# Performance work log

Measured on AMD Instinct MI355X. Metric: run time of the kernel, lower is better.

The kernel has to match this reference:

```python
import jax, jax.numpy as jnp
import numpy as np

DIM = 1024
GROUPS = 32
EPS = 1e-5


def setup_inputs() -> dict:
    key = jax.random.key(0)
    ks = jax.random.split(key, 12)
    b, c, h, w = 16, DIM, 32, 32  # h*w must equal DIM for GroupNorm(32, dim) on (b, hw, c)
    x = jax.random.normal(ks[0], (b, c, h, w), dtype=jnp.float32)
    # GroupNorm affine params: num_channels = dim (applied along hw axis, which == dim)
    gamma = jnp.ones((DIM,), dtype=jnp.float32)
    beta = jnp.zeros((DIM,), dtype=jnp.float32)
    init = lambda k: jax.random.normal(k, (DIM, DIM), dtype=jnp.float32) * 0.02
    Wq, Wk, Wv, Wo = init(ks[1]), init(ks[2]), init(ks[3]), init(ks[4])
    bq = jax.random.normal(ks[5], (DIM,), dtype=jnp.float32) * 0.02
    bk = jax.random.normal(ks[6], (DIM,), dtype=jnp.float32) * 0.02
    bv = jax.random.normal(ks[7], (DIM,), dtype=jnp.float32) * 0.02
    bo = jax.random.normal(ks[8], (DIM,), dtype=jnp.float32) * 0.02
    return {"x": x, "gamma": gamma, "beta": beta,
            "Wq": Wq, "bq": bq, "Wk": Wk, "bk": bk,
            "Wv": Wv, "bv": bv, "Wo": Wo, "bo": bo}


def _group_norm(x, gamma, beta):
    # x: (b, N, c) where N == num_channels (torch GroupNorm normalizes groups along dim 1)
    b, N, c = x.shape
    xg = x.reshape(b, GROUPS, (N // GROUPS) * c)
    mean = xg.mean(-1, keepdims=True)
    var = xg.var(-1, keepdims=True)
    xn = ((xg - mean) * jax.lax.rsqrt(var + EPS)).reshape(b, N, c)
    return xn * gamma[None, :, None] + beta[None, :, None]


def reference(x, gamma, beta, Wq, bq, Wk, bk, Wv, bv, Wo, bo):
    b, c, h, w = x.shape
    xs = x.reshape(b, c, h * w).transpose(0, 2, 1)  # (b, N, c), N = h*w
    norm_x = _group_norm(xs, gamma, beta)
    q = norm_x @ Wq.T + bq
    k = norm_x @ Wk.T + bk
    v = norm_x @ Wv.T + bv
    attn = jnp.einsum('bqd,bkd->bqk', q, k) * (c ** -0.5)
    attn = jax.nn.softmax(attn, axis=-1)
    # Faithful to original: 'bqk,bvd->bqd' sums k and v independently (no contraction between them)
    out = jnp.einsum('bqk,bvd->bqd', attn, v)
    out = out @ Wo.T + bo  # Dropout(p=0.0) is identity
    return out.transpose(0, 2, 1).reshape(b, c, h, w)
```

## Files before the change

### kernel.cpp

```cpp
#include <hip/hip_runtime.h>


#define BATCH 16
#define CH    1024
#define NHW   1024
#define G     32
#define NPG   32
#define EPG   (NPG*CH)
#define EPSV  1e-5f

__global__ __launch_bounds__(256) void k1_fused(
    const float* __restrict__ x, const float* __restrict__ gamma,
    const float* __restrict__ beta, float* __restrict__ colsum)
{
    const int bg = blockIdx.x;
    const int b  = bg >> 5, g = bg & 31;
    const int t  = threadIdx.x;
    const int lane = t & 63, wave = t >> 6;
    const int n4 = t & 7;
    const int c0 = t >> 3;

    __shared__ float pch[CH];
    __shared__ float r1[4], r2[4], rb[4];

    const float4* xg = reinterpret_cast<const float4*>(x + (size_t)b * (CH * NHW) + g * NPG);
    const float4  gm = reinterpret_cast<const float4*>(gamma + g * NPG)[n4];

    float s1 = 0.f, s2 = 0.f;
    for (int ch = c0; ch < CH; ch += 32) {
        float4 v = xg[ch * (NHW / 4) + n4];
        s1 += v.x + v.y + v.z + v.w;
        s2 += v.x * v.x + v.y * v.y + v.z * v.z + v.w * v.w;
        float p = v.x * gm.x + v.y * gm.y + v.z * gm.z + v.w * gm.w;
        p += __shfl_xor(p, 1);
        p += __shfl_xor(p, 2);
        p += __shfl_xor(p, 4);
        if (n4 == 0) pch[ch] = p;
    }
    float bsum = beta[t] + beta[t + 256] + beta[t + 512] + beta[t + 768];
    #pragma unroll
    for (int m = 1; m < 64; m <<= 1) {
        s1 += __shfl_xor(s1, m); s2 += __shfl_xor(s2, m); bsum += __shfl_xor(bsum, m);
    }
    if (lane == 0) { r1[wave] = s1; r2[wave] = s2; rb[wave] = bsum; }
    __syncthreads();

    const float S1 = r1[0] + r1[1] + r1[2] + r1[3];
    const float S2 = r2[0] + r2[1] + r2[2] + r2[3];
    const float SB = rb[0] + rb[1] + rb[2] + rb[3];
    const float mean = S1 * (1.f / EPG);
    const float var  = S2 * (1.f / EPG) - mean * mean;
    const float inv  = rsqrtf(var + EPSV);
    float sg = gm.x + gm.y + gm.z + gm.w;
    sg += __shfl_xor(sg, 1);
    sg += __shfl_xor(sg, 2);
    sg += __shfl_xor(sg, 4);
    const float cshare = SB * (1.f / 32.f) - inv * mean * sg;

    for (int ch = t; ch < CH; ch += 256)
        atomicAdd(&colsum[b * CH + ch], inv * pch[ch] + cshare);
}

__global__ __launch_bounds__(256) void k3_matvec_v(
    const float* __restrict__ Wv, const float* __restrict__ bv,
    const float* __restrict__ colsum, float* __restrict__ S)
{
    const int t = threadIdx.x;
    const int wave = t >> 6, lane = t & 63;
    const int d = blockIdx.x * 4 + wave;
    const float4* wrow = reinterpret_cast<const float4*>(Wv + (size_t)d * CH);
    const float4* cs4  = reinterpret_cast<const float4*>(colsum);
    float acc[BATCH];
    #pragma unroll
    for (int b = 0; b < BATCH; b++) acc[b] = 0.f;
    #pragma unroll
    for (int i = 0; i < 4; i++) {
        int e4 = i * 64 + lane;
        float4 w = wrow[e4];
        #pragma unroll
        for (int b = 0; b < BATCH; b++) {
            float4 c = cs4[b * 256 + e4];
            acc[b] += w.x * c.x + w.y * c.y + w.z * c.z + w.w * c.w;
        }
    }
    #pragma unroll
    for (int b = 0; b < BATCH; b++) {
        float a = acc[b];
        #pragma unroll
        for (int m = 1; m < 64; m <<= 1) a += __shfl_xor(a, m);
        if (lane == 0) S[b * CH + d] = a + (float)NHW * bv[d];
    }
}

__global__ __launch_bounds__(256) void k4_final_bcast(
    const float* __restrict__ Wo, const float* __restrict__ bo,
    const float* __restrict__ S, float* __restrict__ out)
{
    const int t = threadIdx.x;
    const int wave = t >> 6, lane = t & 63;
    const int d = blockIdx.x * 4 + wave;
    const float4* wrow = reinterpret_cast<const float4*>(Wo + (size_t)d * CH);
    const float4* s4   = reinterpret_cast<const float4*>(S);
    float acc[BATCH];
    #pragma unroll
    for (int b = 0; b < BATCH; b++) acc[b] = 0.f;
    #pragma unroll
    for (int i = 0; i < 4; i++) {
        int e4 = i * 64 + lane;
        float4 w = wrow[e4];
        #pragma unroll
        for (int b = 0; b < BATCH; b++) {
            float4 c = s4[b * 256 + e4];
            acc[b] += w.x * c.x + w.y * c.y + w.z * c.z + w.w * c.w;
        }
    }
    #pragma unroll
    for (int b = 0; b < BATCH; b++) {
        #pragma unroll
        for (int m = 1; m < 64; m <<= 1) acc[b] += __shfl_xor(acc[b], m);
    }
    const float bod = bo[d];
    #pragma unroll
    for (int b = 0; b < BATCH; b++) {
        float val = acc[b] + bod;
        float4 v4 = make_float4(val, val, val, val);
        float4* op = reinterpret_cast<float4*>(out + ((size_t)b * CH + d) * NHW);
        #pragma unroll
        for (int i = 0; i < 4; i++) op[i * 64 + lane] = v4;
    }
}

extern "C" void kernel_launch(void* const* d_in, const int* in_sizes, int n_in,
                              void* d_out, int out_size, void* d_ws, size_t ws_size,
                              hipStream_t stream)
{
    const float* x     = (const float*)d_in[0];
    const float* gamma = (const float*)d_in[1];
    const float* beta  = (const float*)d_in[2];
    const float* Wv    = (const float*)d_in[7];
    const float* bv    = (const float*)d_in[8];
    const float* Wo    = (const float*)d_in[9];
    const float* bo    = (const float*)d_in[10];
    float* out = (float*)d_out;

    char* ws = (char*)d_ws;
    float* colsum = (float*)ws;
    float* Sbuf   = (float*)(ws + 65536);

    hipMemsetAsync(colsum, 0, BATCH * CH * sizeof(float), stream);
    k1_fused      <<<BATCH * G, 256, 0, stream>>>(x, gamma, beta, colsum);
    k3_matvec_v   <<<NHW / 4,   256, 0, stream>>>(Wv, bv, colsum, Sbuf);
    k4_final_bcast<<<NHW / 4,   256, 0, stream>>>(Wo, bo, Sbuf, out);
}
```

Baseline: 177.2 us.

## Fuse three kernels into one persistent kernel with grid barriers

Merges the group-norm column-sum, the Wv matvec and the Wo matvec-plus-broadcast into a single 512-block kernel separated by atomic-counter grid barriers, removing two kernel launches and the gaps between them. The work of each later stage is re-split across the 512 blocks: the Wv stage gives each wave 8 batches, and the Wo broadcast stage gives each wave half a row. It relies on all 512 blocks being co-resident, which launch_bounds(256,2) and the CU count must guarantee, otherwise the barrier deadlocks. The barrier spin also adds its own latency.

Measured after the change: 426.1 us. 2.4x slower.

```diff
diff --git a/kernel.cpp b/kernel.cpp
--- a/kernel.cpp
+++ b/kernel.cpp
@@ -8,125 +8,140 @@
 #define NPG   32
 #define EPG   (NPG*CH)
 #define EPSV  1e-5f
+#define GRID  (BATCH*G)
 
-__global__ __launch_bounds__(256) void k1_fused(
-    const float* __restrict__ x, const float* __restrict__ gamma,
-    const float* __restrict__ beta, float* __restrict__ colsum)
+__device__ __forceinline__ void grid_barrier(int* ctr)
 {
-    const int bg = blockIdx.x;
-    const int b  = bg >> 5, g = bg & 31;
-    const int t  = threadIdx.x;
-    const int lane = t & 63, wave = t >> 6;
-    const int n4 = t & 7;
-    const int c0 = t >> 3;
-
-    __shared__ float pch[CH];
-    __shared__ float r1[4], r2[4], rb[4];
-
-    const float4* xg = reinterpret_cast<const float4*>(x + (size_t)b * (CH * NHW) + g * NPG);
-    const float4  gm = reinterpret_cast<const float4*>(gamma + g * NPG)[n4];
-
-    float s1 = 0.f, s2 = 0.f;
-    for (int ch = c0; ch < CH; ch += 32) {
-        float4 v = xg[ch * (NHW / 4) + n4];
-        s1 += v.x + v.y + v.z + v.w;
-        s2 += v.x * v.x + v.y * v.y + v.z * v.z + v.w * v.w;
-        float p = v.x * gm.x + v.y * gm.y + v.z * gm.z + v.w * gm.w;
-        p += __shfl_xor(p, 1);
-        p += __shfl_xor(p, 2);
-        p += __shfl_xor(p, 4);
-        if (n4 == 0) pch[ch] = p;
+    __threadfence();
+    __syncthreads();
+    if (threadIdx.x == 0) {
+        __hip_atomic_fetch_add(ctr, 1, __ATOMIC_RELEASE, __HIP_MEMORY_SCOPE_AGENT);
+        while (__hip_atomic_load(ctr, __ATOMIC_ACQUIRE, __HIP_MEMORY_SCOPE_AGENT) < GRID)
+            __builtin_amdgcn_s_sleep(2);
     }
-    float bsum = beta[t] + beta[t + 256] + beta[t + 512] + beta[t + 768];
-    #pragma unroll
-    for (int m = 1; m < 64; m <<= 1) {
-        s1 += __shfl_xor(s1, m); s2 += __shfl_xor(s2, m); bsum += __shfl_xor(bsum, m);
-    }
-    if (lane == 0) { r1[wave] = s1; r2[wave] = s2; rb[wave] = bsum; }
     __syncthreads();
-
-    const float S1 = r1[0] + r1[1] + r1[2] + r1[3];
-    const float S2 = r2[0] + r2[1] + r2[2] + r2[3];
-    const float SB = rb[0] + rb[1] + rb[2] + rb[3];
-    const float mean = S1 * (1.f / EPG);
-    const float var  = S2 * (1.f / EPG) - mean * mean;
-    const float inv  = rsqrtf(var + EPSV);
-    float sg = gm.x + gm.y + gm.z + gm.w;
-    sg += __shfl_xor(sg, 1);
-    sg += __shfl_xor(sg, 2);
-    sg += __shfl_xor(sg, 4);
-    const float cshare = SB * (1.f / 32.f) - inv * mean * sg;
-
-    for (int ch = t; ch < CH; ch += 256)
-        atomicAdd(&colsum[b * CH + ch], inv * pch[ch] + cshare);
+    __threadfence();
 }
 
-__global__ __launch_bounds__(256) void k3_matvec_v(
+__global__ __launch_bounds__(256, 2) void fused_all(
+    const float* __restrict__ x, const float* __restrict__ gamma,
+    const float* __restrict__ beta,
     const float* __restrict__ Wv, const float* __restrict__ bv,
-    const float* __restrict__ colsum, float* __restrict__ S)
+    const float* __restrict__ Wo, const float* __restrict__ bo,
+    float* __restrict__ colsum, float* __restrict__ S,
+    float* __restrict__ out, int* __restrict__ bar)
 {
-    const int t = threadIdx.x;
-    const int wave = t >> 6, lane = t & 63;
-    const int d = blockIdx.x * 4 + wave;
-    const float4* wrow = reinterpret_cast<const float4*>(Wv + (size_t)d * CH);
-    const float4* cs4  = reinterpret_cast<const float4*>(colsum);
-    float acc[BATCH];
-    #pragma unroll
-    for (int b = 0; b < BATCH; b++) acc[b] = 0.f;
-    #pragma unroll
-    for (int i = 0; i < 4; i++) {
-        int e4 = i * 64 + lane;
-        float4 w = wrow[e4];
+    const int blk  = blockIdx.x;
+    const int t    = threadIdx.x;
+    const int lane = t & 63, wave = t >> 6;
+
+    {
+        const int b  = blk >> 5, g = blk & 31;
+        const int n4 = t & 7;
+        const int c0 = t >> 3;
+        __shared__ float pch[CH];
+        __shared__ float r1[4], r2[4], rb[4];
+
+        const float4* xg = reinterpret_cast<const float4*>(x + (size_t)b * (CH * NHW) + g * NPG);
+        const float4  gm = reinterpret_cast<const float4*>(gamma + g * NPG)[n4];
+
+        float s1 = 0.f, s2 = 0.f;
+        for (int ch = c0; ch < CH; ch += 32) {
+            float4 v = xg[ch * (NHW / 4) + n4];
+            s1 += v.x + v.y + v.z + v.w;
+            s2 += v.x * v.x + v.y * v.y + v.z * v.z + v.w * v.w;
+            float p = v.x * gm.x + v.y * gm.y + v.z * gm.z + v.w * gm.w;
+            p += __shfl_xor(p, 1);
+            p += __shfl_xor(p, 2);
+            p += __shfl_xor(p, 4);
+            if (n4 == 0) pch[ch] = p;
+        }
+        float bsum = beta[t] + beta[t + 256] + beta[t + 512] + beta[t + 768];
+        #pragma unroll
+        for (int m = 1; m < 64; m <<= 1) {
+            s1 += __shfl_xor(s1, m); s2 += __shfl_xor(s2, m); bsum += __shfl_xor(bsum, m);
+        }
+        if (lane == 0) { r1[wave] = s1; r2[wave] = s2; rb[wave] = bsum; }
+        __syncthreads();
+
+        const float S1 = r1[0] + r1[1] + r1[2] + r1[3];
+        const float S2 = r2[0] + r2[1] + r2[2] + r2[3];
+        const float SB = rb[0] + rb[1] + rb[2] + rb[3];
+        const float mean = S1 * (1.f / EPG);
+        const float var  = S2 * (1.f / EPG) - mean * mean;
+        const float inv  = rsqrtf(var + EPSV);
+        float sg = gm.x + gm.y + gm.z + gm.w;
+        sg += __shfl_xor(sg, 1);
+        sg += __shfl_xor(sg, 2);
+        sg += __shfl_xor(sg, 4);
+        const float cshare = SB * (1.f / 32.f) - inv * mean * sg;
+
+        for (int ch = t; ch < CH; ch += 256)
+            atomicAdd(&colsum[b * CH + ch], inv * pch[ch] + cshare);
+    }
+    grid_barrier(&bar[0]);
+
+    {
+        const int d  = blk * 2 + (wave >> 1);
+        const int b0 = (wave & 1) * 8;
+        const float4* wrow = reinterpret_cast<const float4*>(Wv + (size_t)d * CH);
+        const float4* cs4  = reinterpret_cast<const float4*>(colsum);
+        float acc[8];
+        #pragma unroll
+        for (int b = 0; b < 8; b++) acc[b] = 0.f;
+        #pragma unroll
+        for (int i = 0; i < 4; i++) {
+            int e4 = i * 64 + lane;
+            float4 w = wrow[e4];
+            #pragma unroll
+            for (int b = 0; b < 8; b++) {
+                float4 c = cs4[(b0 + b) * 256 + e4];
+                acc[b] += w.x * c.x + w.y * c.y + w.z * c.z + w.w * c.w;
+            }
+        }
+        #pragma unroll
+        for (int b = 0; b < 8; b++) {
+            float a = acc[b];
+            #pragma unroll
+            for (int m = 1; m < 64; m <<= 1) a += __shfl_xor(a, m);
+            if (lane == 0) S[(b0 + b) * CH + d] = a + (float)NHW * bv[d];
+        }
+    }
+    grid_barrier(&bar[1]);
+
+    {
+        const int wid  = blk * 4 + wave;
+        const int d    = wid >> 1;
+        const int half = wid & 1;
+        const float4* wrow = reinterpret_cast<const float4*>(Wo + (size_t)d * CH);
+        const float4* s4   = reinterpret_cast<const float4*>(S);
+        float acc[BATCH];
+        #pragma unroll
+        for (int b = 0; b < BATCH; b++) acc[b] = 0.f;
+        #pragma unroll
+        for (int i = 0; i < 4; i++) {
+            int e4 = i * 64 + lane;
+            float4 w = wrow[e4];
+            #pragma unroll
+            for (int b = 0; b < BATCH; b++) {
+                float4 c = s4[b * 256 + e4];
+                acc[b] += w.x * c.x + w.y * c.y + w.z * c.z + w.w * c.w;
+            }
+        }
         #pragma unroll
         for (int b = 0; b < BATCH; b++) {
-            float4 c = cs4[b * 256 + e4];
-            acc[b] += w.x * c.x + w.y * c.y + w.z * c.z + w.w * c.w;
+            #pragma unroll
+            for (int m = 1; m < 64; m <<= 1) acc[b] += __shfl_xor(acc[b], m);
         }
-    }
-    #pragma unroll
-    for (int b = 0; b < BATCH; b++) {
-        float a = acc[b];
-        #pragma unroll
-        for (int m = 1; m < 64; m <<= 1) a += __shfl_xor(a, m);
-        if (lane == 0) S[b * CH + d] = a + (float)NHW * bv[d];
-    }
-}
-
-__global__ __launch_bounds__(256) void k4_final_bcast(
-    const float* __restrict__ Wo, const float* __restrict__ bo,
-    const float* __restrict__ S, float* __restrict__ out)
-{
-    const int t = threadIdx.x;
-    const int wave = t >> 6, lane = t & 63;
-    const int d = blockIdx.x * 4 + wave;
-    const float4* wrow = reinterpret_cast<const float4*>(Wo + (size_t)d * CH);
-    const float4* s4   = reinterpret_cast<const float4*>(S);
-    float acc[BATCH];
-    #pragma unroll
-    for (int b = 0; b < BATCH; b++) acc[b] = 0.f;
-    #pragma unroll
-    for (int i = 0; i < 4; i++) {
-        int e4 = i * 64 + lane;
-        float4 w = wrow[e4];
+        const float bod = bo[d];
         #pragma unroll
         for (int b = 0; b < BATCH; b++) {
-            float4 c = s4[b * 256 + e4];
-            acc[b] += w.x * c.x + w.y * c.y + w.z * c.z + w.w * c.w;
+            float val = acc[b] + bod;
+            float4 v4 = make_float4(val, val, val, val);
+            float4* op = reinterpret_cast<float4*>(out + ((size_t)b * CH + d) * NHW) + half * 128;
+            #pragma unroll
+            for (int i = 0; i < 2; i++) op[i * 64 + lane] = v4;
         }
-    }
-    #pragma unroll
-    for (int b = 0; b < BATCH; b++) {
-        #pragma unroll
-        for (int m = 1; m < 64; m <<= 1) acc[b] += __shfl_xor(acc[b], m);
-    }
-    const float bod = bo[d];
-    #pragma unroll
-    for (int b = 0; b < BATCH; b++) {
-        float val = acc[b] + bod;
-        float4 v4 = make_float4(val, val, val, val);
-        float4* op = reinterpret_cast<float4*>(out + ((size_t)b * CH + d) * NHW);
-        #pragma unroll
-        for (int i = 0; i < 4; i++) op[i * 64 + lane] = v4;
     }
 }
 
@@ -145,10 +160,10 @@
 
     char* ws = (char*)d_ws;
     float* colsum = (float*)ws;
-    float* Sbuf   = (float*)(ws + 65536);
+    int*   bar    = (int*)(ws + 65536);
+    float* Sbuf   = (float*)(ws + 65536 + 256);
 
-    hipMemsetAsync(colsum, 0, BATCH * CH * sizeof(float), stream);
-    k1_fused      <<<BATCH * G, 256, 0, stream>>>(x, gamma, beta, colsum);
-    k3_matvec_v   <<<NHW / 4,   256, 0, stream>>>(Wv, bv, colsum, Sbuf);
-    k4_final_bcast<<<NHW / 4,   256, 0, stream>>>(Wo, bo, Sbuf, out);
+    hipMemsetAsync(ws, 0, 65536 + 256, stream);
+    fused_all<<<GRID, 256, 0, stream>>>(x, gamma, beta, Wv, bv, Wo, bo,
+                                        colsum, Sbuf, out, bar);
 }
```

## Widen stats and output kernels to 1024 threads with per-batch output blocks

Applied to the files above, without the earlier changes.

The group-stats kernel moves to 1024-thread blocks, and each thread preloads its 8 float4 values into registers before reducing, so more loads are in flight. The output kernel is reorganized so each block handles one batch and a 32-row slab of Wo, staging that batch's S vector in shared memory. This spreads the large broadcast write across 512 blocks instead of 256. The cost is that Wo rows are re-read once per batch instead of once overall, and the 1024-thread blocks carry a minimum-blocks hint that may constrain register allocation.

After: 159.4 us (median of 2 runs). 1.11x faster.

```diff
diff --git a/kernel.cpp b/kernel.cpp
--- a/kernel.cpp
+++ b/kernel.cpp
@@ -9,26 +9,33 @@
 #define EPG   (NPG*CH)
 #define EPSV  1e-5f
 
-__global__ __launch_bounds__(256) void k1_fused(
+__global__ __launch_bounds__(1024, 8) void k1_stats_colsum(
     const float* __restrict__ x, const float* __restrict__ gamma,
     const float* __restrict__ beta, float* __restrict__ colsum)
 {
-    const int bg = blockIdx.x;
-    const int b  = bg >> 5, g = bg & 31;
-    const int t  = threadIdx.x;
+    const int blk  = blockIdx.x;
+    const int t    = threadIdx.x;
     const int lane = t & 63, wave = t >> 6;
-    const int n4 = t & 7;
-    const int c0 = t >> 3;
+    const int b    = blk >> 5, g = blk & 31;
+    const int n4   = t & 7;
+    const int c0   = t >> 3;
 
     __shared__ float pch[CH];
-    __shared__ float r1[4], r2[4], rb[4];
+    __shared__ float r1[16], r2[16], rb[16];
 
     const float4* xg = reinterpret_cast<const float4*>(x + (size_t)b * (CH * NHW) + g * NPG);
     const float4  gm = reinterpret_cast<const float4*>(gamma + g * NPG)[n4];
 
+    float4 vb[8];
+    #pragma unroll
+    for (int k = 0; k < 8; k++)
+        vb[k] = xg[(c0 + k * 128) * (NHW / 4) + n4];
+
     float s1 = 0.f, s2 = 0.f;
-    for (int ch = c0; ch < CH; ch += 32) {
-        float4 v = xg[ch * (NHW / 4) + n4];
+    #pragma unroll
+    for (int k = 0; k < 8; k++) {
+        const float4 v = vb[k];
+        const int ch = c0 + k * 128;
         s1 += v.x + v.y + v.z + v.w;
         s2 += v.x * v.x + v.y * v.y + v.z * v.z + v.w * v.w;
         float p = v.x * gm.x + v.y * gm.y + v.z * gm.z + v.w * gm.w;
@@ -37,7 +44,7 @@
         p += __shfl_xor(p, 4);
         if (n4 == 0) pch[ch] = p;
     }
-    float bsum = beta[t] + beta[t + 256] + beta[t + 512] + beta[t + 768];
+    float bsum = beta[t];
     #pragma unroll
     for (int m = 1; m < 64; m <<= 1) {
         s1 += __shfl_xor(s1, m); s2 += __shfl_xor(s2, m); bsum += __shfl_xor(bsum, m);
@@ -45,9 +52,9 @@
     if (lane == 0) { r1[wave] = s1; r2[wave] = s2; rb[wave] = bsum; }
     __syncthreads();
 
-    const float S1 = r1[0] + r1[1] + r1[2] + r1[3];
-    const float S2 = r2[0] + r2[1] + r2[2] + r2[3];
-    const float SB = rb[0] + rb[1] + rb[2] + rb[3];
+    float S1 = 0.f, S2 = 0.f, SB = 0.f;
+    #pragma unroll
+    for (int w = 0; w < 16; w++) { S1 += r1[w]; S2 += r2[w]; SB += rb[w]; }
     const float mean = S1 * (1.f / EPG);
     const float var  = S2 * (1.f / EPG) - mean * mean;
     const float inv  = rsqrtf(var + EPSV);
@@ -57,11 +64,10 @@
     sg += __shfl_xor(sg, 4);
     const float cshare = SB * (1.f / 32.f) - inv * mean * sg;
 
-    for (int ch = t; ch < CH; ch += 256)
-        atomicAdd(&colsum[b * CH + ch], inv * pch[ch] + cshare);
+    atomicAdd(&colsum[b * CH + t], inv * pch[t] + cshare);
 }
 
-__global__ __launch_bounds__(256) void k3_matvec_v(
+__global__ __launch_bounds__(256) void k2_matvec_v(
     const float* __restrict__ Wv, const float* __restrict__ bv,
     const float* __restrict__ colsum, float* __restrict__ S)
 {
@@ -92,37 +98,38 @@
     }
 }
 
-__global__ __launch_bounds__(256) void k4_final_bcast(
+__global__ __launch_bounds__(1024, 8) void k3_out(
     const float* __restrict__ Wo, const float* __restrict__ bo,
     const float* __restrict__ S, float* __restrict__ out)
 {
-    const int t = threadIdx.x;
-    const int wave = t >> 6, lane = t & 63;
-    const int d = blockIdx.x * 4 + wave;
-    const float4* wrow = reinterpret_cast<const float4*>(Wo + (size_t)d * CH);
-    const float4* s4   = reinterpret_cast<const float4*>(S);
-    float acc[BATCH];
+    const int blk  = blockIdx.x;
+    const int t    = threadIdx.x;
+    const int lane = t & 63, wave = t >> 6;
+    const int b    = blk >> 5, slab = blk & 31;
+
+    __shared__ float smem[CH];
+    if (t < 256)
+        reinterpret_cast<float4*>(smem)[t] =
+            reinterpret_cast<const float4*>(S + (size_t)b * CH)[t];
+    __syncthreads();
+
+    const int d0 = slab * 32 + wave * 2;
+    const float4* s4 = reinterpret_cast<const float4*>(smem);
     #pragma unroll
-    for (int b = 0; b < BATCH; b++) acc[b] = 0.f;
-    #pragma unroll
-    for (int i = 0; i < 4; i++) {
-        int e4 = i * 64 + lane;
-        float4 w = wrow[e4];
+    for (int j = 0; j < 2; j++) {
+        const int d = d0 + j;
+        const float4* wrow = reinterpret_cast<const float4*>(Wo + (size_t)d * CH);
+        float a = 0.f;
         #pragma unroll
-        for (int b = 0; b < BATCH; b++) {
-            float4 c = s4[b * 256 + e4];
-            acc[b] += w.x * c.x + w.y * c.y + w.z * c.z + w.w * c.w;
+        for (int i = 0; i < 4; i++) {
+            int e4 = i * 64 + lane;
+            float4 w = wrow[e4];
+            float4 c = s4[e4];
+            a += w.x * c.x + w.y * c.y + w.z * c.z + w.w * c.w;
         }
-    }
-    #pragma unroll
-    for (int b = 0; b < BATCH; b++) {
         #pragma unroll
-        for (int m = 1; m < 64; m <<= 1) acc[b] += __shfl_xor(acc[b], m);
-    }
-    const float bod = bo[d];
-    #pragma unroll
-    for (int b = 0; b < BATCH; b++) {
-        float val = acc[b] + bod;
+        for (int m = 1; m < 64; m <<= 1) a += __shfl_xor(a, m);
+        const float val = a + bo[d];
         float4 v4 = make_float4(val, val, val, val);
         float4* op = reinterpret_cast<float4*>(out + ((size_t)b * CH + d) * NHW);
         #pragma unroll
@@ -148,7 +155,7 @@
     float* Sbuf   = (float*)(ws + 65536);
 
     hipMemsetAsync(colsum, 0, BATCH * CH * sizeof(float), stream);
-    k1_fused      <<<BATCH * G, 256, 0, stream>>>(x, gamma, beta, colsum);
-    k3_matvec_v   <<<NHW / 4,   256, 0, stream>>>(Wv, bv, colsum, Sbuf);
-    k4_final_bcast<<<NHW / 4,   256, 0, stream>>>(Wo, bo, Sbuf, out);
+    k1_stats_colsum<<<BATCH * G, 1024, 0, stream>>>(x, gamma, beta, colsum);
+    k2_matvec_v    <<<256,       256, 0, stream>>>(Wv, bv, colsum, Sbuf);
+    k3_out         <<<BATCH * G, 1024, 0, stream>>>(Wo, bo, Sbuf, out);
 }
```
